# Optimization experiments

Measured on AMD Instinct MI355X. Metric: run time of the kernel, lower is better.

Reference implementation:

```python
import jax, jax.numpy as jnp
import numpy as np

NUM_HEADS = 4
GROUPS = 16
EPS = 1e-5


def setup_inputs() -> dict:
    key = jax.random.key(0)
    ks = jax.random.split(key, 7)
    b, c, hh, ww = 4, 256, 64, 64
    x = jax.random.normal(ks[0], (b, c, hh, ww), dtype=jnp.float32)
    norm_w = 1.0 + 0.1 * jax.random.normal(ks[1], (c,), dtype=jnp.float32)
    norm_b = 0.1 * jax.random.normal(ks[2], (c,), dtype=jnp.float32)
    qkv_w = jax.random.normal(ks[3], (3 * c, c), dtype=jnp.float32) / np.sqrt(c)
    qkv_b = 0.01 * jax.random.normal(ks[4], (3 * c,), dtype=jnp.float32)
    # NOTE: original zero-inits proj_out; we use random weights so the
    # attention path actually affects the output (kernel correctness test).
    proj_w = jax.random.normal(ks[5], (c, c), dtype=jnp.float32) / np.sqrt(c)
    proj_b = jnp.zeros((c,), dtype=jnp.float32)
    return {"x": x, "norm_w": norm_w, "norm_b": norm_b,
            "qkv_w": qkv_w, "qkv_b": qkv_b,
            "proj_w": proj_w, "proj_b": proj_b}


def _group_norm(x, w, b):
    # x: [B, C, T]; GroupNorm32 computes in fp32 (inputs already fp32)
    B, C, T = x.shape
    xg = x.reshape(B, GROUPS, C // GROUPS, T)
    mean = jnp.mean(xg, axis=(2, 3), keepdims=True)
    var = jnp.var(xg, axis=(2, 3), keepdims=True)
    xn = ((xg - mean) * jax.lax.rsqrt(var + EPS)).reshape(B, C, T)
    return xn * w[None, :, None] + b[None, :, None]


def reference(x, norm_w, norm_b, qkv_w, qkv_b, proj_w, proj_b):
    b, c = x.shape[0], x.shape[1]
    spatial = x.shape[2:]
    x2 = x.reshape(b, c, -1)                       # [B, C, T]
    T = x2.shape[-1]
    normed = _group_norm(x2, norm_w, norm_b)
    qkv = jnp.einsum('oc,bct->bot', qkv_w, normed) + qkv_b[None, :, None]
    # faithful reshape: [B, 3C, T] -> [B*H, 3C/H, T], then split in thirds
    qkv = qkv.reshape(b * NUM_HEADS, (3 * c) // NUM_HEADS, T)
    ch = qkv.shape[1] // 3                         # = C / H
    q, k, v = jnp.split(qkv, 3, axis=1)
    scale = 1.0 / np.sqrt(np.sqrt(ch))
    weight = jnp.einsum('bct,bcs->bts', q * scale, k * scale)
    weight = jax.nn.softmax(weight.astype(jnp.float32), axis=-1).astype(qkv.dtype)
    h = jnp.einsum('bts,bcs->bct', weight, v)      # [B*H, ch, T]
    h = h.reshape(b, c, T)
    h = jnp.einsum('oc,bct->bot', proj_w, h) + proj_b[None, :, None]
    return (x2 + h).reshape(b, c, *spatial)
```

## Files before the change

### kernel.cpp

```cpp
#include <hip/hip_runtime.h>

constexpr int kB  = 4;
constexpr int kC  = 256;
constexpr int kT  = 4096;
constexpr int kG  = 16;
constexpr int kCg = kC / kG;
constexpr int kH  = 4;
constexpr int kCh = kC / kH;
constexpr float kEps = 1e-5f;
constexpr float kQScale = 0.125f * 1.4426950408889634f;

typedef short bf16x8 __attribute__((ext_vector_type(8)));
typedef float f32x4  __attribute__((ext_vector_type(4)));
typedef float f32x16 __attribute__((ext_vector_type(16)));

__device__ inline unsigned short f2bf(float f) {
    union { float f; unsigned u; } v; v.f = f;
    unsigned r = v.u + 0x7fffu + ((v.u >> 16) & 1u);
    return (unsigned short)(r >> 16);
}
__device__ inline unsigned pk2bf(float a, float b) {
    return (unsigned)f2bf(a) | ((unsigned)f2bf(b) << 16);
}
__device__ inline unsigned pk2bf_trunc(float a, float b) {
    return __builtin_amdgcn_perm(__float_as_uint(b), __float_as_uint(a), 0x07060302u);
}
__device__ inline void pls32(unsigned& a, unsigned& b) {
    __asm__("v_permlane32_swap_b32 %0, %1" : "+v"(a), "+v"(b));
}

__global__ __launch_bounds__(256) void prep_kernel(const float* __restrict__ x,
                                                   float* __restrict__ stats,
                                                   const float* __restrict__ qkv_w,
                                                   const float* __restrict__ proj_w,
                                                   unsigned short* __restrict__ wbf) {
    int tid = threadIdx.x;
    if (blockIdx.x >= 64) {
        int gid = (blockIdx.x - 64) * 256 + tid;
        for (int i = gid; i < 65536; i += 128 * 256) {
            float4 v = (i < 49152) ? ((const float4*)qkv_w)[i]
                                   : ((const float4*)proj_w)[i - 49152];
            *(uint2*)&wbf[(size_t)i * 4] = make_uint2(pk2bf(v.x, v.y), pk2bf(v.z, v.w));
        }
        return;
    }
    int bg = blockIdx.x;
    const float4* xp4 = (const float4*)(x + (size_t)bg * (kCg * kT));
    float s = 0.f, q = 0.f;
    #pragma unroll 4
    for (int i = 0; i < (kCg * kT / 4) / 256; ++i) {
        float4 v = xp4[tid + i * 256];
        s += v.x + v.y + v.z + v.w;
        q += v.x * v.x + v.y * v.y + v.z * v.z + v.w * v.w;
    }
    #pragma unroll
    for (int off = 32; off > 0; off >>= 1) {
        s += __shfl_down(s, off);
        q += __shfl_down(q, off);
    }
    __shared__ float rs[4], rq[4];
    int wid = tid >> 6, lane = tid & 63;
    if (lane == 0) { rs[wid] = s; rq[wid] = q; }
    __syncthreads();
    if (tid == 0) {
        float S = rs[0] + rs[1] + rs[2] + rs[3];
        float Q = rq[0] + rq[1] + rq[2] + rq[3];
        const float invN = 1.0f / (float)(kCg * kT);
        float mean = S * invN;
        float var  = Q * invN - mean * mean;
        stats[bg * 2 + 0] = mean;
        stats[bg * 2 + 1] = rsqrtf(var + kEps);
    }
}

__global__ __launch_bounds__(256) void gn_apply_t_kernel(const float* __restrict__ x,
                                                         const float* __restrict__ stats,
                                                         const float* __restrict__ w,
                                                         const float* __restrict__ bias,
                                                         unsigned short* __restrict__ normT) {
    __shared__ float Ls[64][65];
    int t0 = blockIdx.x * 64;
    int c0 = blockIdx.y * 64;
    int b  = blockIdx.z;
    int tid = threadIdx.x;
    #pragma unroll
    for (int p = 0; p < 4; ++p) {
        int idx = tid + p * 256;
        int cl = idx >> 4, t4 = idx & 15;
        int c = c0 + cl;
        int bg = b * kG + (c >> 4);
        float mean = stats[bg * 2 + 0];
        float rstd = stats[bg * 2 + 1];
        float sw = w[c] * rstd;
        float sb = bias[c] - mean * sw;
        float4 v = *(const float4*)&x[((size_t)b * kC + c) * kT + t0 + t4 * 4];
        Ls[t4 * 4 + 0][cl] = v.x * sw + sb;
        Ls[t4 * 4 + 1][cl] = v.y * sw + sb;
        Ls[t4 * 4 + 2][cl] = v.z * sw + sb;
        Ls[t4 * 4 + 3][cl] = v.w * sw + sb;
    }
    __syncthreads();
    {
        int row = tid >> 2, cq = (tid & 3) * 16;
        unsigned tmp[8];
        #pragma unroll
        for (int i = 0; i < 8; ++i)
            tmp[i] = pk2bf(Ls[row][cq + 2 * i], Ls[row][cq + 2 * i + 1]);
        uint4* dst = (uint4*)&normT[((size_t)b * kT + t0 + row) * kC + c0 + cq];
        dst[0] = make_uint4(tmp[0], tmp[1], tmp[2], tmp[3]);
        dst[1] = make_uint4(tmp[4], tmp[5], tmp[6], tmp[7]);
    }
}

__global__ __launch_bounds__(256) void qkv_gemm_kernel(const unsigned short* __restrict__ wbf,
                                                       const float* __restrict__ qkv_b,
                                                       const unsigned short* __restrict__ normT,
                                                       unsigned short* __restrict__ qTg,
                                                       unsigned short* __restrict__ kTg,
                                                       unsigned short* __restrict__ vCg) {
    constexpr int LDK = 72;
    constexpr int LDV = 136;
    __shared__ __align__(16) unsigned short As[64 * LDK];
    __shared__ __align__(16) unsigned short Bs[128 * LDK];

    int t0 = blockIdx.x * 128;
    int m0 = blockIdx.y * 64;
    int b  = blockIdx.z;
    const unsigned short* Ab = wbf + (size_t)m0 * kC;
    const unsigned short* Bb = normT + (size_t)b * kT * kC;

    int tid = threadIdx.x;
    int wave = tid >> 6, lane = tid & 63;
    int ln15 = lane & 15, quad = lane >> 4;
    int wm = wave >> 1, wt = wave & 1;

    f32x4 acc[2][4] = {};

    for (int k0 = 0; k0 < kC; k0 += 64) {
        __syncthreads();
        #pragma unroll
        for (int p = 0; p < 2; ++p) {
            int idx = tid + p * 256;
            int row = idx >> 3, seg = idx & 7;
            *(uint4*)&As[row * LDK + seg * 8] =
                *(const uint4*)&Ab[(size_t)row * kC + k0 + seg * 8];
        }
        #pragma unroll
        for (int p = 0; p < 4; ++p) {
            int idx = tid + p * 256;
            int row = idx >> 3, seg = idx & 7;
            *(uint4*)&Bs[row * LDK + seg * 8] =
                *(const uint4*)&Bb[(size_t)(t0 + row) * kC + k0 + seg * 8];
        }
        __syncthreads();
        #pragma unroll
        for (int ks = 0; ks < 2; ++ks) {
            bf16x8 af[2], bf[4];
            #pragma unroll
            for (int i = 0; i < 2; ++i)
                af[i] = *(bf16x8*)&As[(wm * 32 + i * 16 + ln15) * LDK + ks * 32 + quad * 8];
            #pragma unroll
            for (int j = 0; j < 4; ++j)
                bf[j] = *(bf16x8*)&Bs[(wt * 64 + j * 16 + ln15) * LDK + ks * 32 + quad * 8];
            #pragma unroll
            for (int i = 0; i < 2; ++i)
                #pragma unroll
                for (int j = 0; j < 4; ++j)
                    acc[i][j] = __builtin_amdgcn_mfma_f32_16x16x32_bf16(
                        af[i], bf[j], acc[i][j], 0, 0, 0);
        }
    }

    int type = (m0 % 192) / 64;
    int h = m0 / 192;
    int bh = b * kH + h;
    __syncthreads();
    #pragma unroll
    for (int i = 0; i < 2; ++i) {
        float4 bv = *(const float4*)&qkv_b[m0 + wm * 32 + i * 16 + quad * 4];
        const float* bp = (const float*)&bv;
        #pragma unroll
        for (int j = 0; j < 4; ++j) {
            int tl = wt * 64 + j * 16 + ln15;
            int c = wm * 32 + i * 16 + quad * 4;
            float v0 = acc[i][j][0] + bp[0];
            float v1 = acc[i][j][1] + bp[1];
            float v2 = acc[i][j][2] + bp[2];
            float v3 = acc[i][j][3] + bp[3];
            if (type == 0) {
                v0 *= kQScale; v1 *= kQScale; v2 *= kQScale; v3 *= kQScale;
            }
            if (type != 2) {
                *(uint2*)&Bs[tl * LDK + c] = make_uint2(pk2bf(v0, v1), pk2bf(v2, v3));
            } else {
                Bs[(c + 0) * LDV + tl] = f2bf(v0);
                Bs[(c + 1) * LDV + tl] = f2bf(v1);
                Bs[(c + 2) * LDV + tl] = f2bf(v2);
                Bs[(c + 3) * LDV + tl] = f2bf(v3);
            }
        }
    }
    __syncthreads();
    if (type != 2) {
        unsigned short* base = ((type == 0) ? qTg : kTg) + (size_t)bh * (kT * kCh);
        #pragma unroll
        for (int p = 0; p < 4; ++p) {
            int f = tid + p * 256;
            int ln = f & 31, hif = (f >> 5) & 1, ks = (f >> 6) & 3, tb = f >> 8;
            *(uint4*)&base[((t0 >> 5) + tb) * 2048 + ks * 512 + hif * 256 + ln * 8] =
                *(uint4*)&Bs[(tb * 32 + ln) * LDK + ks * 16 + hif * 8];
        }
    } else {
        unsigned short* base = vCg + (size_t)bh * (kT * kCh);
        #pragma unroll
        for (int p = 0; p < 4; ++p) {
            int f = tid + p * 256;
            int c = f & 63, hif = (f >> 6) & 1, sg = f >> 7;
            *(uint4*)&base[((t0 >> 4) + sg) * 1024 + hif * 512 + c * 8] =
                *(uint4*)&Bs[c * LDV + sg * 16 + hif * 8];
        }
    }
}

__global__ __launch_bounds__(256, 4) void attn_mfma_kernel(const unsigned short* __restrict__ qTg,
                                                           const unsigned short* __restrict__ kTg,
                                                           const unsigned short* __restrict__ vCg,
                                                           unsigned short* __restrict__ attnT) {
    __shared__ float Ored[2][32][64];
    __shared__ float Lred[2][64];

    int bh = blockIdx.y;
    int t0 = blockIdx.x * 64;
    int b = bh >> 2, h = bh & 3;

    int tid = threadIdx.x;
    int wave = tid >> 6, lane = tid & 63;
    int ln31 = lane & 31, hi = lane >> 5;
    int tc = wave & 1;
    int sh = wave >> 1;

    const unsigned short* qb = qTg + (size_t)bh * (kT * kCh);
    const unsigned short* kb = kTg + (size_t)bh * (kT * kCh);
    const unsigned short* vb = vCg + (size_t)bh * (kT * kCh);

    bf16x8 qf[4];
    {
        const unsigned short* qp = qb + ((size_t)(t0 >> 5) + tc) * 2048 + hi * 256 + ln31 * 8;
        #pragma unroll
        for (int ks = 0; ks < 4; ++ks) qf[ks] = *(const bf16x8*)(qp + ks * 512);
    }

    const unsigned short* kp = kb + (size_t)sh * 131072 + hi * 256 + ln31 * 8;
    const unsigned short* vp = vb + (size_t)sh * 131072 + hi * 512 + ln31 * 8;

    float l_r = 0.f;
    f32x16 accO0 = {}, accO1 = {};
    union PunP { uint4 u; bf16x8 f; };

    #pragma unroll 1
    for (int it = 0; it < 64; ++it) {
        bf16x8 kf0 = *(const bf16x8*)(kp);
        bf16x8 kf1 = *(const bf16x8*)(kp + 512);
        bf16x8 kf2 = *(const bf16x8*)(kp + 1024);
        bf16x8 kf3 = *(const bf16x8*)(kp + 1536);
        bf16x8 vf00 = *(const bf16x8*)(vp);
        bf16x8 vf10 = *(const bf16x8*)(vp + 256);
        bf16x8 vf01 = *(const bf16x8*)(vp + 1024);
        bf16x8 vf11 = *(const bf16x8*)(vp + 1024 + 256);
        kp += 2048; vp += 2048;

        f32x16 accS = {};
        accS = __builtin_amdgcn_mfma_f32_32x32x16_bf16(kf0, qf[0], accS, 0, 0, 0);
        accS = __builtin_amdgcn_mfma_f32_32x32x16_bf16(kf1, qf[1], accS, 0, 0, 0);
        accS = __builtin_amdgcn_mfma_f32_32x32x16_bf16(kf2, qf[2], accS, 0, 0, 0);
        accS = __builtin_amdgcn_mfma_f32_32x32x16_bf16(kf3, qf[3], accS, 0, 0, 0);

        unsigned u00, u01, u10, u11, u20, u21, u30, u31;
        {
            float p0 = __builtin_amdgcn_exp2f(accS[0]);
            float p1 = __builtin_amdgcn_exp2f(accS[1]);
            float p2 = __builtin_amdgcn_exp2f(accS[2]);
            float p3 = __builtin_amdgcn_exp2f(accS[3]);
            l_r += (p0 + p1) + (p2 + p3);
            u00 = pk2bf_trunc(p0, p1); u01 = pk2bf_trunc(p2, p3);
        }
        {
            float p0 = __builtin_amdgcn_exp2f(accS[4]);
            float p1 = __builtin_amdgcn_exp2f(accS[5]);
            float p2 = __builtin_amdgcn_exp2f(accS[6]);
            float p3 = __builtin_amdgcn_exp2f(accS[7]);
            l_r += (p0 + p1) + (p2 + p3);
            u10 = pk2bf_trunc(p0, p1); u11 = pk2bf_trunc(p2, p3);
        }
        {
            float p0 = __builtin_amdgcn_exp2f(accS[8]);
            float p1 = __builtin_amdgcn_exp2f(accS[9]);
            float p2 = __builtin_amdgcn_exp2f(accS[10]);
            float p3 = __builtin_amdgcn_exp2f(accS[11]);
            l_r += (p0 + p1) + (p2 + p3);
            u20 = pk2bf_trunc(p0, p1); u21 = pk2bf_trunc(p2, p3);
        }
        {
            float p0 = __builtin_amdgcn_exp2f(accS[12]);
            float p1 = __builtin_amdgcn_exp2f(accS[13]);
            float p2 = __builtin_amdgcn_exp2f(accS[14]);
            float p3 = __builtin_amdgcn_exp2f(accS[15]);
            l_r += (p0 + p1) + (p2 + p3);
            u30 = pk2bf_trunc(p0, p1); u31 = pk2bf_trunc(p2, p3);
        }

        pls32(u00, u10);
        pls32(u01, u11);
        pls32(u20, u30);
        pls32(u21, u31);
        PunP F0, F1;
        F0.u = make_uint4(u00, u01, u10, u11);
        F1.u = make_uint4(u20, u21, u30, u31);

        accO0 = __builtin_amdgcn_mfma_f32_32x32x16_bf16(vf00, F0.f, accO0, 0, 0, 0);
        accO1 = __builtin_amdgcn_mfma_f32_32x32x16_bf16(vf10, F0.f, accO1, 0, 0, 0);
        accO0 = __builtin_amdgcn_mfma_f32_32x32x16_bf16(vf01, F1.f, accO0, 0, 0, 0);
        accO1 = __builtin_amdgcn_mfma_f32_32x32x16_bf16(vf11, F1.f, accO1, 0, 0, 0);
    }

    l_r += __shfl_xor(l_r, 32);

    if (sh == 1) {
        #pragma unroll
        for (int e = 0; e < 16; ++e) {
            Ored[tc][e][lane]      = accO0[e];
            Ored[tc][16 + e][lane] = accO1[e];
        }
        Lred[tc][lane] = l_r;
    }
    __syncthreads();
    if (sh == 0) {
        #pragma unroll
        for (int e = 0; e < 16; ++e) {
            accO0[e] += Ored[tc][e][lane];
            accO1[e] += Ored[tc][16 + e][lane];
        }
        l_r += Lred[tc][lane];
        float linv = 1.0f / l_r;
        int t = t0 + tc * 32 + ln31;
        #pragma unroll
        for (int ct = 0; ct < 2; ++ct) {
            const f32x16& ao = ct ? accO1 : accO0;
            #pragma unroll
            for (int g = 0; g < 4; ++g) {
                int c = h * kCh + ct * 32 + 8 * g + 4 * hi;
                float v0 = ao[4 * g + 0] * linv;
                float v1 = ao[4 * g + 1] * linv;
                float v2 = ao[4 * g + 2] * linv;
                float v3 = ao[4 * g + 3] * linv;
                *(uint2*)&attnT[((size_t)b * kT + t) * kC + c] =
                    make_uint2(pk2bf(v0, v1), pk2bf(v2, v3));
            }
        }
    }
}

__global__ __launch_bounds__(256) void proj_gemm_kernel(const unsigned short* __restrict__ wpbf,
                                                        const float* __restrict__ proj_b,
                                                        const unsigned short* __restrict__ attnT,
                                                        const float* __restrict__ x,
                                                        float* __restrict__ out) {
    constexpr int LDK = 72;
    __shared__ __align__(16) unsigned short As[64 * LDK];
    __shared__ __align__(16) unsigned short Bs[128 * LDK];

    int t0 = blockIdx.x * 128;
    int m0 = blockIdx.y * 64;
    int b  = blockIdx.z;
    const unsigned short* Ab = wpbf + (size_t)m0 * kC;
    const unsigned short* Bb = attnT + (size_t)b * kT * kC;

    int tid = threadIdx.x;
    int wave = tid >> 6, lane = tid & 63;
    int ln15 = lane & 15, quad = lane >> 4;
    int wm = wave >> 1, wt = wave & 1;

    f32x4 acc[2][4] = {};

    for (int k0 = 0; k0 < kC; k0 += 64) {
        __syncthreads();
        #pragma unroll
        for (int p = 0; p < 2; ++p) {
            int idx = tid + p * 256;
            int row = idx >> 3, seg = idx & 7;
            *(uint4*)&As[row * LDK + seg * 8] =
                *(const uint4*)&Ab[(size_t)row * kC + k0 + seg * 8];
        }
        #pragma unroll
        for (int p = 0; p < 4; ++p) {
            int idx = tid + p * 256;
            int row = idx >> 3, seg = idx & 7;
            *(uint4*)&Bs[row * LDK + seg * 8] =
                *(const uint4*)&Bb[(size_t)(t0 + row) * kC + k0 + seg * 8];
        }
        __syncthreads();
        #pragma unroll
        for (int ks = 0; ks < 2; ++ks) {
            bf16x8 af[2], bf[4];
            #pragma unroll
            for (int i = 0; i < 2; ++i)
                af[i] = *(bf16x8*)&As[(wm * 32 + i * 16 + ln15) * LDK + ks * 32 + quad * 8];
            #pragma unroll
            for (int j = 0; j < 4; ++j)
                bf[j] = *(bf16x8*)&Bs[(wt * 64 + j * 16 + ln15) * LDK + ks * 32 + quad * 8];
            #pragma unroll
            for (int i = 0; i < 2; ++i)
                #pragma unroll
                for (int j = 0; j < 4; ++j)
                    acc[i][j] = __builtin_amdgcn_mfma_f32_16x16x32_bf16(
                        af[i], bf[j], acc[i][j], 0, 0, 0);
        }
    }

    #pragma unroll
    for (int i = 0; i < 2; ++i) {
        float4 bv = *(const float4*)&proj_b[m0 + wm * 32 + i * 16 + quad * 4];
        const float* bp = (const float*)&bv;
        #pragma unroll
        for (int j = 0; j < 4; ++j) {
            int t = t0 + wt * 64 + j * 16 + ln15;
            int mbase = m0 + wm * 32 + i * 16 + quad * 4;
            #pragma unroll
            for (int r = 0; r < 4; ++r) {
                size_t off = ((size_t)b * kC + mbase + r) * kT + t;
                out[off] = acc[i][j][r] + bp[r] + x[off];
            }
        }
    }
}

extern "C" void kernel_launch(void* const* d_in, const int* in_sizes, int n_in,
                              void* d_out, int out_size, void* d_ws, size_t ws_size,
                              hipStream_t stream) {
    const float* x      = (const float*)d_in[0];
    const float* norm_w = (const float*)d_in[1];
    const float* norm_b = (const float*)d_in[2];
    const float* qkv_w  = (const float*)d_in[3];
    const float* qkv_b  = (const float*)d_in[4];
    const float* proj_w = (const float*)d_in[5];
    const float* proj_b = (const float*)d_in[6];
    float* out = (float*)d_out;

    float* stats = (float*)d_ws;
    unsigned short* wsbf  = (unsigned short*)((float*)d_ws + 128);
    unsigned short* normT = wsbf;
    unsigned short* wbf   = normT + (size_t)kB * kT * kC;
    unsigned short* qTp   = wbf + 262144;
    unsigned short* kTp   = qTp + (size_t)kB * kH * kT * kCh;
    unsigned short* vCp   = kTp + (size_t)kB * kH * kT * kCh;
    unsigned short* attnT = vCp + (size_t)kB * kH * kT * kCh;
    unsigned short* wpbf  = wbf + 196608;

    prep_kernel<<<192, 256, 0, stream>>>(x, stats, qkv_w, proj_w, wbf);
    gn_apply_t_kernel<<<dim3(kT / 64, kC / 64, kB), 256, 0, stream>>>(
        x, stats, norm_w, norm_b, normT);
    qkv_gemm_kernel<<<dim3(kT / 128, 12, kB), 256, 0, stream>>>(
        wbf, qkv_b, normT, qTp, kTp, vCp);
    attn_mfma_kernel<<<dim3(kT / 64, kB * kH), 256, 0, stream>>>(qTp, kTp, vCp, attnT);
    proj_gemm_kernel<<<dim3(kT / 128, kC / 64, kB), 256, 0, stream>>>(
        wpbf, proj_b, attnT, x, out);
}
```

Measured before the change: 212.6 us.

## Process two query tiles per wave with double-buffered K/V loads in attention

Each attention block now covers 128 queries instead of 64. Every wave holds two 32-query Q fragments, so each K/V fragment loaded from global memory is reused for twice the MFMA work. K/V loads are software-pipelined across two register sets, s_setprio is raised around the MFMA sections, and block IDs are remapped so neighbouring blocks in launch order fall in different heads. The cost is more registers: launch bounds drop from 4 to 2 blocks per SIMD, the grid is halved to 512 blocks, and the shared reduction buffers double, which may reduce latency hiding.

```diff
diff --git a/kernel.cpp b/kernel.cpp
--- a/kernel.cpp
+++ b/kernel.cpp
@@ -222,15 +222,17 @@
     }
 }
 
-__global__ __launch_bounds__(256, 4) void attn_mfma_kernel(const unsigned short* __restrict__ qTg,
+__global__ __launch_bounds__(256, 2) void attn_mfma_kernel(const unsigned short* __restrict__ qTg,
                                                            const unsigned short* __restrict__ kTg,
                                                            const unsigned short* __restrict__ vCg,
                                                            unsigned short* __restrict__ attnT) {
-    __shared__ float Ored[2][32][64];
-    __shared__ float Lred[2][64];
-
-    int bh = blockIdx.y;
-    int t0 = blockIdx.x * 64;
+    __shared__ float Ored[2][2][32][64];
+    __shared__ float Lred[2][2][64];
+
+    int lid = blockIdx.y * 32 + blockIdx.x;
+    int wl  = (lid & 7) * 64 + (lid >> 3);
+    int bh  = wl >> 5;
+    int t0  = (wl & 31) * 128;
     int b = bh >> 2, h = bh & 3;
 
     int tid = threadIdx.x;
@@ -243,118 +245,154 @@
     const unsigned short* kb = kTg + (size_t)bh * (kT * kCh);
     const unsigned short* vb = vCg + (size_t)bh * (kT * kCh);
 
-    bf16x8 qf[4];
+    bf16x8 qA[4], qB[4];
     {
-        const unsigned short* qp = qb + ((size_t)(t0 >> 5) + tc) * 2048 + hi * 256 + ln31 * 8;
-        #pragma unroll
-        for (int ks = 0; ks < 4; ++ks) qf[ks] = *(const bf16x8*)(qp + ks * 512);
-    }
-
-    const unsigned short* kp = kb + (size_t)sh * 131072 + hi * 256 + ln31 * 8;
-    const unsigned short* vp = vb + (size_t)sh * 131072 + hi * 512 + ln31 * 8;
-
-    float l_r = 0.f;
-    f32x16 accO0 = {}, accO1 = {};
+        const unsigned short* qp = qb + ((size_t)(t0 >> 5) + tc * 2) * 2048 + hi * 256 + ln31 * 8;
+        #pragma unroll
+        for (int ks = 0; ks < 4; ++ks) {
+            qA[ks] = *(const bf16x8*)(qp + ks * 512);
+            qB[ks] = *(const bf16x8*)(qp + 2048 + ks * 512);
+        }
+    }
+
+    const unsigned short* kbase = kb + (size_t)sh * 131072 + hi * 256 + ln31 * 8;
+    const unsigned short* vbase = vb + (size_t)sh * 131072 + hi * 512 + ln31 * 8;
+
+    float lA = 0.f, lB = 0.f;
+    f32x16 oA0 = {}, oA1 = {}, oB0 = {}, oB1 = {};
     union PunP { uint4 u; bf16x8 f; };
 
-    #pragma unroll 1
-    for (int it = 0; it < 64; ++it) {
-        bf16x8 kf0 = *(const bf16x8*)(kp);
-        bf16x8 kf1 = *(const bf16x8*)(kp + 512);
-        bf16x8 kf2 = *(const bf16x8*)(kp + 1024);
-        bf16x8 kf3 = *(const bf16x8*)(kp + 1536);
-        bf16x8 vf00 = *(const bf16x8*)(vp);
-        bf16x8 vf10 = *(const bf16x8*)(vp + 256);
-        bf16x8 vf01 = *(const bf16x8*)(vp + 1024);
-        bf16x8 vf11 = *(const bf16x8*)(vp + 1024 + 256);
-        kp += 2048; vp += 2048;
-
-        f32x16 accS = {};
-        accS = __builtin_amdgcn_mfma_f32_32x32x16_bf16(kf0, qf[0], accS, 0, 0, 0);
-        accS = __builtin_amdgcn_mfma_f32_32x32x16_bf16(kf1, qf[1], accS, 0, 0, 0);
-        accS = __builtin_amdgcn_mfma_f32_32x32x16_bf16(kf2, qf[2], accS, 0, 0, 0);
-        accS = __builtin_amdgcn_mfma_f32_32x32x16_bf16(kf3, qf[3], accS, 0, 0, 0);
-
+    auto loadKV = [&](bf16x8* kf, bf16x8* vf, int idx) {
+        const unsigned short* kp = kbase + (size_t)idx * 2048;
+        const unsigned short* vp = vbase + (size_t)idx * 2048;
+        kf[0] = *(const bf16x8*)(kp);
+        kf[1] = *(const bf16x8*)(kp + 512);
+        kf[2] = *(const bf16x8*)(kp + 1024);
+        kf[3] = *(const bf16x8*)(kp + 1536);
+        vf[0] = *(const bf16x8*)(vp);
+        vf[1] = *(const bf16x8*)(vp + 256);
+        vf[2] = *(const bf16x8*)(vp + 1024);
+        vf[3] = *(const bf16x8*)(vp + 1280);
+    };
+
+    auto softmax_pack = [&](const f32x16& s, float& l, bf16x8& f0, bf16x8& f1) {
         unsigned u00, u01, u10, u11, u20, u21, u30, u31;
         {
-            float p0 = __builtin_amdgcn_exp2f(accS[0]);
-            float p1 = __builtin_amdgcn_exp2f(accS[1]);
-            float p2 = __builtin_amdgcn_exp2f(accS[2]);
-            float p3 = __builtin_amdgcn_exp2f(accS[3]);
-            l_r += (p0 + p1) + (p2 + p3);
+            float p0 = __builtin_amdgcn_exp2f(s[0]);
+            float p1 = __builtin_amdgcn_exp2f(s[1]);
+            float p2 = __builtin_amdgcn_exp2f(s[2]);
+            float p3 = __builtin_amdgcn_exp2f(s[3]);
+            l += (p0 + p1) + (p2 + p3);
             u00 = pk2bf_trunc(p0, p1); u01 = pk2bf_trunc(p2, p3);
         }
         {
-            float p0 = __builtin_amdgcn_exp2f(accS[4]);
-            float p1 = __builtin_amdgcn_exp2f(accS[5]);
-            float p2 = __builtin_amdgcn_exp2f(accS[6]);
-            float p3 = __builtin_amdgcn_exp2f(accS[7]);
-            l_r += (p0 + p1) + (p2 + p3);
+            float p0 = __builtin_amdgcn_exp2f(s[4]);
+            float p1 = __builtin_amdgcn_exp2f(s[5]);
+            float p2 = __builtin_amdgcn_exp2f(s[6]);
+            float p3 = __builtin_amdgcn_exp2f(s[7]);
+            l += (p0 + p1) + (p2 + p3);
             u10 = pk2bf_trunc(p0, p1); u11 = pk2bf_trunc(p2, p3);
         }
         {
-            float p0 = __builtin_amdgcn_exp2f(accS[8]);
-            float p1 = __builtin_amdgcn_exp2f(accS[9]);
-            float p2 = __builtin_amdgcn_exp2f(accS[10]);
-            float p3 = __builtin_amdgcn_exp2f(accS[11]);
-            l_r += (p0 + p1) + (p2 + p3);
+            float p0 = __builtin_amdgcn_exp2f(s[8]);
+            float p1 = __builtin_amdgcn_exp2f(s[9]);
+            float p2 = __builtin_amdgcn_exp2f(s[10]);
+            float p3 = __builtin_amdgcn_exp2f(s[11]);
+            l += (p0 + p1) + (p2 + p3);
             u20 = pk2bf_trunc(p0, p1); u21 = pk2bf_trunc(p2, p3);
         }
         {
-            float p0 = __builtin_amdgcn_exp2f(accS[12]);
-            float p1 = __builtin_amdgcn_exp2f(accS[13]);
-            float p2 = __builtin_amdgcn_exp2f(accS[14]);
-            float p3 = __builtin_amdgcn_exp2f(accS[15]);
-            l_r += (p0 + p1) + (p2 + p3);
+            float p0 = __builtin_amdgcn_exp2f(s[12]);
+            float p1 = __builtin_amdgcn_exp2f(s[13]);
+            float p2 = __builtin_amdgcn_exp2f(s[14]);
+            float p3 = __builtin_amdgcn_exp2f(s[15]);
+            l += (p0 + p1) + (p2 + p3);
             u30 = pk2bf_trunc(p0, p1); u31 = pk2bf_trunc(p2, p3);
         }
-
-        pls32(u00, u10);
-        pls32(u01, u11);
-        pls32(u20, u30);
-        pls32(u21, u31);
-        PunP F0, F1;
-        F0.u = make_uint4(u00, u01, u10, u11);
-        F1.u = make_uint4(u20, u21, u30, u31);
-
-        accO0 = __builtin_amdgcn_mfma_f32_32x32x16_bf16(vf00, F0.f, accO0, 0, 0, 0);
-        accO1 = __builtin_amdgcn_mfma_f32_32x32x16_bf16(vf10, F0.f, accO1, 0, 0, 0);
-        accO0 = __builtin_amdgcn_mfma_f32_32x32x16_bf16(vf01, F1.f, accO0, 0, 0, 0);
-        accO1 = __builtin_amdgcn_mfma_f32_32x32x16_bf16(vf11, F1.f, accO1, 0, 0, 0);
-    }
-
-    l_r += __shfl_xor(l_r, 32);
+        pls32(u00, u10); pls32(u01, u11);
+        pls32(u20, u30); pls32(u21, u31);
+        PunP P0, P1;
+        P0.u = make_uint4(u00, u01, u10, u11);
+        P1.u = make_uint4(u20, u21, u30, u31);
+        f0 = P0.f; f1 = P1.f;
+    };
+
+    auto computeTile = [&](const bf16x8* kf, const bf16x8* vf) {
+        f32x16 sA = {}, sB = {};
+        __builtin_amdgcn_s_setprio(1);
+        #pragma unroll
+        for (int ks = 0; ks < 4; ++ks) {
+            sA = __builtin_amdgcn_mfma_f32_32x32x16_bf16(kf[ks], qA[ks], sA, 0, 0, 0);
+            sB = __builtin_amdgcn_mfma_f32_32x32x16_bf16(kf[ks], qB[ks], sB, 0, 0, 0);
+        }
+        __builtin_amdgcn_s_setprio(0);
+        bf16x8 FA0, FA1, FB0, FB1;
+        softmax_pack(sA, lA, FA0, FA1);
+        softmax_pack(sB, lB, FB0, FB1);
+        __builtin_amdgcn_s_setprio(1);
+        oA0 = __builtin_amdgcn_mfma_f32_32x32x16_bf16(vf[0], FA0, oA0, 0, 0, 0);
+        oA1 = __builtin_amdgcn_mfma_f32_32x32x16_bf16(vf[1], FA0, oA1, 0, 0, 0);
+        oB0 = __builtin_amdgcn_mfma_f32_32x32x16_bf16(vf[0], FB0, oB0, 0, 0, 0);
+        oB1 = __builtin_amdgcn_mfma_f32_32x32x16_bf16(vf[1], FB0, oB1, 0, 0, 0);
+        oA0 = __builtin_amdgcn_mfma_f32_32x32x16_bf16(vf[2], FA1, oA0, 0, 0, 0);
+        oA1 = __builtin_amdgcn_mfma_f32_32x32x16_bf16(vf[3], FA1, oA1, 0, 0, 0);
+        oB0 = __builtin_amdgcn_mfma_f32_32x32x16_bf16(vf[2], FB1, oB0, 0, 0, 0);
+        oB1 = __builtin_amdgcn_mfma_f32_32x32x16_bf16(vf[3], FB1, oB1, 0, 0, 0);
+        __builtin_amdgcn_s_setprio(0);
+    };
+
+    bf16x8 kX[4], vX[4], kY[4], vY[4];
+    loadKV(kX, vX, 0);
+    #pragma unroll 1
+    for (int it = 0; it < 64; it += 2) {
+        loadKV(kY, vY, it + 1);
+        computeTile(kX, vX);
+        loadKV(kX, vX, (it + 2) & 63);
+        computeTile(kY, vY);
+    }
+
+    lA += __shfl_xor(lA, 32);
+    lB += __shfl_xor(lB, 32);
 
     if (sh == 1) {
         #pragma unroll
         for (int e = 0; e < 16; ++e) {
-            Ored[tc][e][lane]      = accO0[e];
-            Ored[tc][16 + e][lane] = accO1[e];
-        }
-        Lred[tc][lane] = l_r;
+            Ored[tc][0][e][lane]      = oA0[e];
+            Ored[tc][0][16 + e][lane] = oA1[e];
+            Ored[tc][1][e][lane]      = oB0[e];
+            Ored[tc][1][16 + e][lane] = oB1[e];
+        }
+        Lred[tc][0][lane] = lA;
+        Lred[tc][1][lane] = lB;
     }
     __syncthreads();
     if (sh == 0) {
         #pragma unroll
         for (int e = 0; e < 16; ++e) {
-            accO0[e] += Ored[tc][e][lane];
-            accO1[e] += Ored[tc][16 + e][lane];
-        }
-        l_r += Lred[tc][lane];
-        float linv = 1.0f / l_r;
-        int t = t0 + tc * 32 + ln31;
-        #pragma unroll
-        for (int ct = 0; ct < 2; ++ct) {
-            const f32x16& ao = ct ? accO1 : accO0;
-            #pragma unroll
-            for (int g = 0; g < 4; ++g) {
-                int c = h * kCh + ct * 32 + 8 * g + 4 * hi;
-                float v0 = ao[4 * g + 0] * linv;
-                float v1 = ao[4 * g + 1] * linv;
-                float v2 = ao[4 * g + 2] * linv;
-                float v3 = ao[4 * g + 3] * linv;
-                *(uint2*)&attnT[((size_t)b * kT + t) * kC + c] =
-                    make_uint2(pk2bf(v0, v1), pk2bf(v2, v3));
+            oA0[e] += Ored[tc][0][e][lane];
+            oA1[e] += Ored[tc][0][16 + e][lane];
+            oB0[e] += Ored[tc][1][e][lane];
+            oB1[e] += Ored[tc][1][16 + e][lane];
+        }
+        lA += Lred[tc][0][lane];
+        lB += Lred[tc][1][lane];
+        #pragma unroll
+        for (int ch = 0; ch < 2; ++ch) {
+            float linv = 1.0f / (ch ? lB : lA);
+            int t = t0 + tc * 64 + ch * 32 + ln31;
+            #pragma unroll
+            for (int ct = 0; ct < 2; ++ct) {
+                const f32x16& ao = ch ? (ct ? oB1 : oB0) : (ct ? oA1 : oA0);
+                #pragma unroll
+                for (int g = 0; g < 4; ++g) {
+                    int c = h * kCh + ct * 32 + 8 * g + 4 * hi;
+                    float v0 = ao[4 * g + 0] * linv;
+                    float v1 = ao[4 * g + 1] * linv;
+                    float v2 = ao[4 * g + 2] * linv;
+                    float v3 = ao[4 * g + 3] * linv;
+                    *(uint2*)&attnT[((size_t)b * kT + t) * kC + c] =
+                        make_uint2(pk2bf(v0, v1), pk2bf(v2, v3));
+                }
             }
         }
     }
@@ -461,7 +499,7 @@
         x, stats, norm_w, norm_b, normT);
     qkv_gemm_kernel<<<dim3(kT / 128, 12, kB), 256, 0, stream>>>(
         wbf, qkv_b, normT, qTp, kTp, vCp);
-    attn_mfma_kernel<<<dim3(kT / 64, kB * kH), 256, 0, stream>>>(qTp, kTp, vCp, attnT);
+    attn_mfma_kernel<<<dim3(kT / 128, kB * kH), 256, 0, stream>>>(qTp, kTp, vCp, attnT);
     proj_gemm_kernel<<<dim3(kT / 128, kC / 64, kB), 256, 0, stream>>>(
         wpbf, proj_b, attnT, x, out);
 }
```

Measured after the change: 195.7 us. -8.0%, faster.
